# Kernel tuning notes

Hardware: AMD Instinct MI355X
Metric: run time of the kernel (lower is better)

Reference implementation:

```python
import jax, jax.numpy as jnp
import numpy as np

H, DH = 8, 40                      # heads, dim_head
SCALE = DH ** -0.5
NEG = -3.4028235e38                # -finfo(float32).max
EMBDIM, STEPS, EMBEDS = 512, 1000, 50


def _gelu(x):
    return jax.nn.gelu(x, approximate=False)  # torch.nn.GELU default (erf)


def setup_inputs() -> dict:
    key = jax.random.key(0)
    ks = jax.random.split(key, 16)
    b, i, j = 16, 4096, 77
    qd, cd, inner = 320, 768, 320
    s = lambda k, sh, f: jax.random.normal(k, sh, jnp.float32) * f
    bc2 = jnp.tile(jnp.array([0.0, -3.0], jnp.float32), H)  # INITBIAS on class 1
    return dict(
        x=jax.random.normal(ks[0], (b, i, qd), jnp.float32),
        embs=jax.random.normal(ks[1], (b, j, cd), jnp.float32),
        cam=jax.random.uniform(ks[2], (b, i, j), jnp.float32),
        progress=jax.random.uniform(ks[3], (b,), jnp.float32),
        strength=jnp.float32(1.0),
        Wq=s(ks[4], (qd, inner), qd ** -0.5),
        Wk=s(ks[5], (cd, inner), cd ** -0.5),
        Wv=s(ks[6], (cd, inner), cd ** -0.5),
        Wo=s(ks[7], (inner, qd), inner ** -0.5),
        bo=jnp.zeros((qd,), jnp.float32),
        emb1=s(ks[8], (EMBEDS + 1, EMBDIM), 1.0),
        emb2=s(ks[9], (STEPS // EMBEDS, EMBDIM), 1.0),
        Wc1=s(ks[10], (EMBDIM, EMBDIM), EMBDIM ** -0.5),
        bc1=jnp.zeros((EMBDIM,), jnp.float32),
        Wc2=s(ks[11], (EMBDIM, 2 * H), EMBDIM ** -0.5),
        bc2=bc2,
        captiontypes=jax.random.randint(ks[12], (b, j), 0, 5),
    )


def reference(x, embs, cam, progress, strength, Wq, Wk, Wv, Wo, bo,
              emb1, emb2, Wc1, bc1, Wc2, bc2, captiontypes):
    b, i, _ = x.shape
    j = embs.shape[1]
    # projections, split heads: 'b n (h d) -> (b h) n d'
    q = (x @ Wq).reshape(b, i, H, DH).transpose(0, 2, 1, 3).reshape(b * H, i, DH)
    k = (embs @ Wk).reshape(b, j, H, DH).transpose(0, 2, 1, 3).reshape(b * H, j, DH)
    v = (embs @ Wv).reshape(b, j, H, DH).transpose(0, 2, 1, 3).reshape(b * H, j, DH)
    # fp32 QK^T (fp32 already)
    sim = jnp.einsum('bid,bjd->bij', q.astype(jnp.float32), k.astype(jnp.float32))

    # cross_attention_control (CustomCrossAttentionMinimal)
    mask2 = jnp.repeat((captiontypes >= 2)[:, None, :], H, axis=0)  # [(bh),1,j]
    # weight_func under no_grad: std of sim where captiontypes>=2 (unbiased)
    sim_sg = jax.lax.stop_gradient(sim)
    mfull = jnp.broadcast_to(mask2, sim.shape)
    n = mfull.sum().astype(jnp.float32)
    mean = jnp.sum(jnp.where(mfull, sim_sg, 0.0)) / n
    var = jnp.sum(jnp.where(mfull, (sim_sg - mean) ** 2, 0.0)) / (n - 1.0)
    simstd = jnp.sqrt(var)
    wf = jax.lax.stop_gradient(cam * simstd * strength)        # [b,i,j]
    wf = jnp.repeat(wf[:, None], H, axis=1).reshape(b * H, i, j)
    wf = jnp.where(mask2, wf, 0.0)
    useglobal = wf.sum(-1) == 0                                 # [(bh),i]
    wfmax = wf.max(-1, keepdims=True)
    wfb = wf >= (jnp.maximum(wfmax, 0.001) - 0.0001)            # bool [(bh),i,j]
    gmask = jnp.repeat(((captiontypes >= 0) & (captiontypes < 2))[:, None, :], H, axis=0)
    lmask = wfb | (useglobal[:, :, None] & gmask)
    gattn = jax.nn.softmax(jnp.where(gmask, sim, NEG) * SCALE, axis=-1)
    lattn = jax.nn.softmax(jnp.where(lmask, sim, NEG) * SCALE, axis=-1)

    # ProgressClassifier: DiscretizedProgressEmbed -> GELU -> Linear -> GELU -> Linear
    xstep = jnp.minimum(jnp.round(progress * STEPS).astype(jnp.int32), STEPS - 1)
    per = STEPS // EMBEDS  # 20
    e = emb1[xstep // per] + emb2[xstep % per]                  # [b, 512]
    e = _gelu(_gelu(e) @ Wc1 + bc1)
    logits = e @ Wc2 + bc2                                      # [b, 2H]
    pc = jax.nn.softmax(logits.reshape(b, H, 2), axis=-1).reshape(b * H, 2)

    attn = gattn * pc[:, 0, None, None] + lattn * pc[:, 1, None, None]
    out = jnp.einsum('bij,bjd->bid', attn, v.astype(jnp.float32))
    out = out.reshape(b, H, i, DH).transpose(0, 2, 1, 3).reshape(b, i, H * DH)
    return out @ Wo + bo
```

## Files before the change

### kernel.cpp

```cpp
#include <hip/hip_runtime.h>


typedef _Float16 vh8 __attribute__((ext_vector_type(8)));
typedef _Float16 vh4 __attribute__((ext_vector_type(4)));
typedef float    vf4 __attribute__((ext_vector_type(4)));

#define NEGBIG  (-3.4028235e38f)
#define SCALE_F 0.15811388300841897f
#define INFF    (__builtin_inff())

__device__ __forceinline__ vh8 h8zero() {
  vh8 v;
#pragma unroll
  for (int i = 0; i < 8; ++i) v[i] = (_Float16)0.f;
  return v;
}
__device__ __forceinline__ vf4 f4zero() {
  vf4 v;
#pragma unroll
  for (int i = 0; i < 4; ++i) v[i] = 0.f;
  return v;
}
__device__ __forceinline__ float gelu_exact(float x) {
  return 0.5f * x * (1.0f + erff(x * 0.70710678118654752f));
}
__device__ __forceinline__ unsigned swzA(int row) {
  return (unsigned)(((row & 7) << 4) ^ (((row >> 3) & 1) << 5));
}
__device__ __forceinline__ unsigned swzB(int row) {
  return (unsigned)((row & 7) << 4);
}
__device__ __forceinline__ void glds16(const void* g, void* l) {
  __builtin_amdgcn_global_load_lds((const __attribute__((address_space(1))) unsigned*)g,
                                   (__attribute__((address_space(3))) unsigned*)l, 16, 0, 0);
}

__global__ __launch_bounds__(256) void transpose_kernel(
    const float* __restrict__ Wq, const float* __restrict__ Wk,
    const float* __restrict__ Wv, const float* __restrict__ Wo,
    _Float16* __restrict__ WqT, _Float16* __restrict__ WkvT, _Float16* __restrict__ WoT)
{
  __shared__ float ts[32][33];
  int tile = blockIdx.x;
  const float* src; _Float16* dst; int dstK, rowOff;
  if (tile < 100)      { src = Wq; dst = WqT;  dstK = 320; rowOff = 0; }
  else if (tile < 340) { src = Wk; dst = WkvT; dstK = 768; rowOff = 0;   tile -= 100; }
  else if (tile < 580) { src = Wv; dst = WkvT; dstK = 768; rowOff = 320; tile -= 340; }
  else                 { src = Wo; dst = WoT;  dstK = 320; rowOff = 0;   tile -= 580; }
  int kb = tile / 10, nb = tile - kb * 10;
  int k0 = kb * 32, n0 = nb * 32;
  int r = threadIdx.x >> 5, c = threadIdx.x & 31;
#pragma unroll
  for (int p = 0; p < 4; ++p)
    ts[r + p * 8][c] = src[(size_t)(k0 + r + p * 8) * 320 + n0 + c];
  __syncthreads();
#pragma unroll
  for (int p = 0; p < 4; ++p)
    dst[(size_t)(rowOff + n0 + r + p * 8) * dstK + k0 + c] = (_Float16)ts[c][r + p * 8];
}

__global__ __launch_bounds__(256) void vtrans_kernel(
    const _Float16* __restrict__ vf, unsigned* __restrict__ vTg32)
{
  const int b = blockIdx.x, h = blockIdx.y, t = threadIdx.x;
  unsigned* out = vTg32 + (size_t)(b * 8 + h) * 3072;
#pragma unroll
  for (int p = 0; p < 12; ++p) {
    int idx = t + p * 256;
    int d = idx >> 6;
    int u = idx & 63;
    int c = u >> 2, pr = u & 3;
    int sd = (int)(swzA(d) >> 4);
    int j0 = ((c ^ sd) << 3) + pr * 2;
    unsigned lo = 0, hi = 0;
    if (d < 40) {
      if (j0 < 77)     lo = *(const unsigned short*)(vf + (size_t)(b * 77 + j0) * 640 + h * 40 + d);
      if (j0 + 1 < 77) hi = *(const unsigned short*)(vf + (size_t)(b * 77 + j0 + 1) * 640 + h * 40 + d);
    }
    out[idx] = lo | (hi << 16);
  }
}

__global__ __launch_bounds__(256) void kv_gemm_kernel(
    const float* __restrict__ Ap, const _Float16* __restrict__ Bt,
    _Float16* __restrict__ Cp)
{
  const int t = threadIdx.x, lane = t & 63, wave = t >> 6;
  const int m0 = blockIdx.x * 64;
  const int n0 = blockIdx.y * 160;
  const int l15 = lane & 15, l4 = lane >> 4;
  const int rg = wave >> 1, cg = wave & 1;

  vf4 acc[2][5];
#pragma unroll
  for (int a = 0; a < 2; ++a)
#pragma unroll
    for (int bq = 0; bq < 5; ++bq) acc[a][bq] = f4zero();

#pragma unroll 2
  for (int kk = 0; kk < 24; ++kk) {
    int k = kk * 32 + l4 * 8;
    vh8 av[2];
#pragma unroll
    for (int mt = 0; mt < 2; ++mt) {
      int row = m0 + rg * 32 + mt * 16 + l15;
      av[mt] = h8zero();
      if (row < 1232) {
        const float* ap = Ap + (size_t)row * 768 + k;
        float4 f0 = *(const float4*)ap;
        float4 f1 = *(const float4*)(ap + 4);
        vh8 hv;
        hv[0] = (_Float16)f0.x; hv[1] = (_Float16)f0.y; hv[2] = (_Float16)f0.z; hv[3] = (_Float16)f0.w;
        hv[4] = (_Float16)f1.x; hv[5] = (_Float16)f1.y; hv[6] = (_Float16)f1.z; hv[7] = (_Float16)f1.w;
        av[mt] = hv;
      }
    }
#pragma unroll
    for (int nt = 0; nt < 5; ++nt) {
      int n = n0 + cg * 80 + nt * 16 + l15;
      vh8 bv = *(const vh8*)(Bt + (size_t)n * 768 + k);
      acc[0][nt] = __builtin_amdgcn_mfma_f32_16x16x32_f16(av[0], bv, acc[0][nt], 0, 0, 0);
      acc[1][nt] = __builtin_amdgcn_mfma_f32_16x16x32_f16(av[1], bv, acc[1][nt], 0, 0, 0);
    }
  }
#pragma unroll
  for (int mt = 0; mt < 2; ++mt)
#pragma unroll
    for (int nt = 0; nt < 5; ++nt) {
      int n = n0 + cg * 80 + nt * 16 + l15;
#pragma unroll
      for (int r = 0; r < 4; ++r) {
        int m = m0 + rg * 32 + mt * 16 + l4 * 4 + r;
        if (m < 1232) Cp[(size_t)m * 640 + n] = (_Float16)acc[mt][nt][r];
      }
    }
}

__global__ __launch_bounds__(512) void qproj_kernel(
    const float* __restrict__ x, const _Float16* __restrict__ Bt,
    const _Float16* __restrict__ kf, const int* __restrict__ ctypes,
    _Float16* __restrict__ qhm, double* __restrict__ partials)
{
  __shared__ __align__(16) char smem[81920];
  const int t = threadIdx.x, lane = t & 63, wave = t >> 6;
  const int m0 = blockIdx.x * 128;
  const int l15 = lane & 15, l4 = lane >> 4;
  const int wbase = t & ~63;
  const int rg = wave >> 1, cg = wave & 1;
  const float* arow0 = x + (size_t)(m0 + rg * 16 + l15) * 320 + l4 * 8;
  const float* arow1 = x + (size_t)(m0 + 64 + rg * 16 + l15) * 320 + l4 * 8;

  vf4 acc[2][10];
#pragma unroll
  for (int s = 0; s < 2; ++s)
#pragma unroll
    for (int bq = 0; bq < 10; ++bq) acc[s][bq] = f4zero();

  float4 fA[8], fB[8];

#pragma unroll
  for (int p = 0; p < 5; ++p) {
    int idx = t + p * 512;
    int n = idx >> 3, c8 = idx & 7;
    glds16(Bt + (size_t)n * 320 + ((c8 ^ (n & 7)) << 3),
           smem + (size_t)(p * 512 + wbase) * 16);
  }
#pragma unroll
  for (int ks = 0; ks < 2; ++ks) {
    fA[0 + ks * 2 + 0] = *(const float4*)(arow0 + ks * 32);
    fA[0 + ks * 2 + 1] = *(const float4*)(arow0 + ks * 32 + 4);
    fA[4 + ks * 2 + 0] = *(const float4*)(arow1 + ks * 32);
    fA[4 + ks * 2 + 1] = *(const float4*)(arow1 + ks * 32 + 4);
  }
  __syncthreads();

#pragma unroll
  for (int kc = 0; kc < 5; ++kc) {
    char* BsCur = smem + (size_t)(kc & 1) * 40960;
    if (kc < 4) {
      int k0n = (kc + 1) * 64;
      char* BsNxt = smem + (size_t)((kc + 1) & 1) * 40960;
#pragma unroll
      for (int p = 0; p < 5; ++p) {
        int idx = t + p * 512;
        int n = idx >> 3, c8 = idx & 7;
        glds16(Bt + (size_t)n * 320 + k0n + ((c8 ^ (n & 7)) << 3),
               BsNxt + (size_t)(p * 512 + wbase) * 16);
      }
      float4* nxt = (kc & 1) ? fA : fB;
#pragma unroll
      for (int ks = 0; ks < 2; ++ks) {
        nxt[0 + ks * 2 + 0] = *(const float4*)(arow0 + k0n + ks * 32);
        nxt[0 + ks * 2 + 1] = *(const float4*)(arow0 + k0n + ks * 32 + 4);
        nxt[4 + ks * 2 + 0] = *(const float4*)(arow1 + k0n + ks * 32);
        nxt[4 + ks * 2 + 1] = *(const float4*)(arow1 + k0n + ks * 32 + 4);
      }
    }
    float4* cur = (kc & 1) ? fB : fA;
#pragma unroll
    for (int s = 0; s < 2; ++s) {
#pragma unroll
      for (int ks = 0; ks < 2; ++ks) {
        float4 f0 = cur[s * 4 + ks * 2 + 0];
        float4 f1 = cur[s * 4 + ks * 2 + 1];
        vh8 av;
        av[0] = (_Float16)f0.x; av[1] = (_Float16)f0.y; av[2] = (_Float16)f0.z; av[3] = (_Float16)f0.w;
        av[4] = (_Float16)f1.x; av[5] = (_Float16)f1.y; av[6] = (_Float16)f1.z; av[7] = (_Float16)f1.w;
#pragma unroll
        for (int nt = 0; nt < 10; ++nt) {
          int n = cg * 160 + nt * 16 + l15;
          unsigned byte = (unsigned)(n * 128 + (ks * 32 + l4 * 8) * 2) ^ swzB(n);
          vh8 bv = *(const vh8*)(BsCur + byte);
          acc[s][nt] = __builtin_amdgcn_mfma_f32_16x16x32_f16(av, bv, acc[s][nt], 0, 0, 0);
        }
      }
    }
    __syncthreads();
  }

  double S = 0.0, S2 = 0.0;
  const int b = m0 >> 12;
  const int h = wave;
#pragma unroll
  for (int s = 0; s < 2; ++s) {
#pragma unroll
    for (int nt = 0; nt < 10; ++nt) {
      int col = cg * 160 + nt * 16 + l15;
#pragma unroll
      for (int r = 0; r < 4; ++r) {
        int lr = rg * 16 + l4 * 4 + r;
        unsigned byte = (unsigned)(lr * 640 + col * 2) ^ swzB(lr);
        *(_Float16*)(smem + byte) = (_Float16)acc[s][nt][r];
      }
    }
    __syncthreads();
#pragma unroll
    for (int p = 0; p < 5; ++p) {
      int idx = t + p * 512;
      int hh = idx / 320;
      int rem = idx - hh * 320;
      int lrow = rem / 5;
      int c = rem - lrow * 5;
      unsigned sb = (unsigned)(lrow * 640 + hh * 80 + c * 16) ^ swzB(lrow);
      vh8 v = *(const vh8*)(smem + sb);
      int gi = m0 + s * 64 + lrow;
      int bb = gi >> 12, ii = gi & 4095;
      *(vh8*)(qhm + ((size_t)(bb * 8 + hh) * 4096 + ii) * 40 + c * 8) = v;
    }
    {
      vh8 a0v[4], a1v[4];
#pragma unroll
      for (int mt = 0; mt < 4; ++mt) {
        int qrow = mt * 16 + l15;
        unsigned b0 = (unsigned)(qrow * 640 + (h * 40 + l4 * 8) * 2) ^ swzB(qrow);
        a0v[mt] = *(const vh8*)(smem + b0);
        a1v[mt] = h8zero();
        if (l4 == 0) {
          unsigned b1 = (unsigned)(qrow * 640 + (h * 40 + 32) * 2) ^ swzB(qrow);
          a1v[mt] = *(const vh8*)(smem + b1);
        }
      }
#pragma unroll
      for (int jt = 0; jt < 5; ++jt) {
        int j = jt * 16 + l15;
        bool valid = (j < 77);
        vh8 b0 = h8zero(), b1 = h8zero();
        int ctj = -1;
        if (valid) {
          const _Float16* kp = kf + (size_t)(b * 77 + j) * 640 + h * 40;
          b0 = *(const vh8*)(kp + l4 * 8);
          if (l4 == 0) b1 = *(const vh8*)(kp + 32);
          ctj = ctypes[b * 77 + j];
        }
#pragma unroll
        for (int mt = 0; mt < 4; ++mt) {
          vf4 sv4 = f4zero();
          sv4 = __builtin_amdgcn_mfma_f32_16x16x32_f16(a0v[mt], b0, sv4, 0, 0, 0);
          sv4 = __builtin_amdgcn_mfma_f32_16x16x32_f16(a1v[mt], b1, sv4, 0, 0, 0);
          if (ctj >= 2) {
#pragma unroll
            for (int r = 0; r < 4; ++r) {
              double sv = (double)sv4[r];
              S += sv; S2 += sv * sv;
            }
          }
        }
      }
    }
    __syncthreads();
  }
#pragma unroll
  for (int off = 32; off > 0; off >>= 1) {
    S += __shfl_xor(S, off);
    S2 += __shfl_xor(S2, off);
  }
  if (lane == 0) {
    int idx = blockIdx.x * 8 + wave;
    partials[2 * idx + 0] = S;
    partials[2 * idx + 1] = S2;
  }
}

__global__ __launch_bounds__(512) void oproj_kernel(
    const _Float16* __restrict__ hohm, const _Float16* __restrict__ Bt,
    const float* __restrict__ bias, float* __restrict__ out)
{
  __shared__ __align__(16) _Float16 Bs[2][320 * 64];
  const int t = threadIdx.x, lane = t & 63, wave = t >> 6;
  const int m0 = blockIdx.x * 128;
  const int l15 = lane & 15, l4 = lane >> 4;
  const int wbase = t & ~63;
  const int rg = wave >> 1, cg = wave & 1;

  const int gi0 = m0 + rg * 16 + l15;
  const int gi1 = gi0 + 64;
  const int bb0 = gi0 >> 12, ii0 = gi0 & 4095;
  const int bb1 = gi1 >> 12, ii1 = gi1 & 4095;

  vf4 acc[2][10];
#pragma unroll
  for (int s = 0; s < 2; ++s)
#pragma unroll
    for (int bq = 0; bq < 10; ++bq) acc[s][bq] = f4zero();

  vh8 hA[4], hB[4];

#pragma unroll
  for (int p = 0; p < 5; ++p) {
    int idx = t + p * 512;
    int n = idx >> 3, c8 = idx & 7;
    glds16(Bt + (size_t)n * 320 + ((c8 ^ (n & 7)) << 3),
           (char*)Bs[0] + (size_t)(p * 512 + wbase) * 16);
  }
#pragma unroll
  for (int ks = 0; ks < 2; ++ks) {
    int k = ks * 32 + l4 * 8;
    int hh = k / 40, d = k - hh * 40;
    hA[0 + ks] = *(const vh8*)(hohm + ((size_t)(bb0 * 8 + hh) * 4096 + ii0) * 40 + d);
    hA[2 + ks] = *(const vh8*)(hohm + ((size_t)(bb1 * 8 + hh) * 4096 + ii1) * 40 + d);
  }
  __syncthreads();

#pragma unroll
  for (int kc = 0; kc < 5; ++kc) {
    const char* BsCur = (const char*)Bs[kc & 1];
    if (kc < 4) {
      int k0n = (kc + 1) * 64;
      char* BsNxt = (char*)Bs[(kc + 1) & 1];
#pragma unroll
      for (int p = 0; p < 5; ++p) {
        int idx = t + p * 512;
        int n = idx >> 3, c8 = idx & 7;
        glds16(Bt + (size_t)n * 320 + k0n + ((c8 ^ (n & 7)) << 3),
               BsNxt + (size_t)(p * 512 + wbase) * 16);
      }
      vh8* nxt = (kc & 1) ? hA : hB;
#pragma unroll
      for (int ks = 0; ks < 2; ++ks) {
        int k = k0n + ks * 32 + l4 * 8;
        int hh = k / 40, d = k - hh * 40;
        nxt[0 + ks] = *(const vh8*)(hohm + ((size_t)(bb0 * 8 + hh) * 4096 + ii0) * 40 + d);
        nxt[2 + ks] = *(const vh8*)(hohm + ((size_t)(bb1 * 8 + hh) * 4096 + ii1) * 40 + d);
      }
    }
    vh8* cur = (kc & 1) ? hB : hA;
#pragma unroll
    for (int s = 0; s < 2; ++s) {
#pragma unroll
      for (int ks = 0; ks < 2; ++ks) {
#pragma unroll
        for (int nt = 0; nt < 10; ++nt) {
          int n = cg * 160 + nt * 16 + l15;
          unsigned byte = (unsigned)(n * 128 + (ks * 32 + l4 * 8) * 2) ^ swzB(n);
          vh8 bv = *(const vh8*)(BsCur + byte);
          acc[s][nt] = __builtin_amdgcn_mfma_f32_16x16x32_f16(cur[s * 2 + ks], bv, acc[s][nt], 0, 0, 0);
        }
      }
    }
    __syncthreads();
  }
#pragma unroll
  for (int s = 0; s < 2; ++s)
#pragma unroll
    for (int nt = 0; nt < 10; ++nt) {
      int n = cg * 160 + nt * 16 + l15;
      float bias_v = bias[n];
#pragma unroll
      for (int r = 0; r < 4; ++r) {
        int m = m0 + s * 64 + rg * 16 + l4 * 4 + r;
        out[(size_t)m * 320 + n] = acc[s][nt][r] + bias_v;
      }
    }
}

__global__ __launch_bounds__(256) void classifier_kernel(
    const float* __restrict__ progress,
    const float* __restrict__ emb1, const float* __restrict__ emb2,
    const float* __restrict__ Wc1, const float* __restrict__ bc1,
    const float* __restrict__ Wc2, const float* __restrict__ bc2,
    float* __restrict__ pcb)
{
  __shared__ float g[512];
  __shared__ float h1[512];
  __shared__ float lg[16];
  const int b = blockIdx.x;
  const int t = threadIdx.x;

  float pr = progress[b];
  int xstep = (int)rintf(pr * 1000.0f);
  if (xstep > 999) xstep = 999;
  int a = xstep / 20;
  int r = xstep - a * 20;

  for (int d = t; d < 512; d += 256) {
    float e = emb1[a * 512 + d] + emb2[r * 512 + d];
    g[d] = gelu_exact(e);
  }
  __syncthreads();
  for (int n = t; n < 512; n += 256) {
    float acc = bc1[n];
    for (int d = 0; d < 512; ++d) acc = fmaf(g[d], Wc1[d * 512 + n], acc);
    h1[n] = gelu_exact(acc);
  }
  __syncthreads();
  if (t < 16) {
    float acc = bc2[t];
    for (int d = 0; d < 512; ++d) acc = fmaf(h1[d], Wc2[d * 16 + t], acc);
    lg[t] = acc;
  }
  __syncthreads();
  if (t < 8) {
    float a0 = lg[2 * t], a1 = lg[2 * t + 1];
    float mx = fmaxf(a0, a1);
    float e0 = __expf(a0 - mx), e1 = __expf(a1 - mx);
    float inv = 1.0f / (e0 + e1);
    pcb[(b * 8 + t) * 2 + 0] = e0 * inv;
    pcb[(b * 8 + t) * 2 + 1] = e1 * inv;
  }
}

__global__ __launch_bounds__(256) void finalize_kernel(
    const double* __restrict__ partials, const int* __restrict__ ctypes,
    float* __restrict__ ssb)
{
  __shared__ double rs[256];
  __shared__ double rs2[256];
  __shared__ int rc[256];
  const int t = threadIdx.x;
  double S = 0.0, S2 = 0.0;
#pragma unroll
  for (int p = 0; p < 16; ++p) {
    int idx = t + p * 256;
    S += partials[2 * idx + 0];
    S2 += partials[2 * idx + 1];
  }
  int c = 0;
#pragma unroll
  for (int p = 0; p < 5; ++p) {
    int idx = t + p * 256;
    if (idx < 1232) c += (ctypes[idx] >= 2) ? 1 : 0;
  }
  rs[t] = S; rs2[t] = S2; rc[t] = c;
  __syncthreads();
  for (int off = 128; off > 0; off >>= 1) {
    if (t < off) { rs[t] += rs[t + off]; rs2[t] += rs2[t + off]; rc[t] += rc[t + off]; }
    __syncthreads();
  }
  if (t == 0) {
    double n = (double)rc[0] * 8.0 * 4096.0;
    double mean = rs[0] / n;
    double var = (rs2[0] - n * mean * mean) / (n - 1.0);
    ssb[0] = (float)sqrt(var > 0.0 ? var : 0.0);
  }
}

__global__ __launch_bounds__(256) void lmask_kernel(
    const float* __restrict__ cam, const int* __restrict__ ctypes,
    const float* __restrict__ ssb, const float* __restrict__ strengthp,
    unsigned* __restrict__ lmp)
{
  __shared__ float camt[64 * 81];
  __shared__ unsigned char gmv[96];
  __shared__ unsigned char m2v[96];
  const int t = threadIdx.x;
  const int it = blockIdx.x, b = blockIdx.y;
  const int i0 = it * 64;

  if (t < 96) {
    int j = t;
    int ct = (j < 77) ? ctypes[b * 77 + j] : -1;
    gmv[j] = (j < 77 && ct >= 0 && ct < 2) ? 1 : 0;
    m2v[j] = (j < 77 && ct >= 2) ? 1 : 0;
  }
#pragma unroll
  for (int p = 0; p < 20; ++p) {
    int idx = t + p * 256;
    int row = idx / 80;
    int j = idx - row * 80;
    camt[row * 81 + j] = (j < 77) ? cam[((size_t)b * 4096 + i0 + row) * 77 + j] : 0.f;
  }
  __syncthreads();

  const float ss = ssb[0];
  const float st = strengthp[0];
  int row = t >> 2, qd = t & 3;
  float wfv[20];
  float wmax = 0.f, wsum = 0.f;
#pragma unroll
  for (int m = 0; m < 20; ++m) {
    int j = qd + 4 * m;
    float wf = 0.f;
    if (j < 77 && m2v[j]) wf = (camt[row * 81 + j] * ss) * st;
    wfv[m] = wf;
    wmax = fmaxf(wmax, wf);
    wsum += wf;
  }
  wmax = fmaxf(wmax, __shfl_xor(wmax, 1));
  wmax = fmaxf(wmax, __shfl_xor(wmax, 2));
  wsum += __shfl_xor(wsum, 1);
  wsum += __shfl_xor(wsum, 2);
  float thr = fmaxf(wmax, 0.001f) - 0.0001f;
  bool ug = (wsum == 0.f);
  unsigned wbits = 0u;
#pragma unroll
  for (int m = 0; m < 20; ++m) {
    int j = qd + 4 * m;
    bool lv = (wfv[m] >= thr) || (ug && (j < 77) && gmv[j]);
    if (lv) wbits |= (1u << m);
  }
  lmp[((size_t)b * 4096 + i0 + row) * 4 + qd] = wbits;
}

__global__ __launch_bounds__(256) void attn_kernel(
    const _Float16* __restrict__ qhm, const _Float16* __restrict__ kf,
    const unsigned* __restrict__ vTg32, const int* __restrict__ ctypes,
    const float* __restrict__ pcb, const unsigned* __restrict__ lmp,
    _Float16* __restrict__ hohm)
{
  __shared__ _Float16 vT[48 * 128];
  __shared__ _Float16 attnbuf[64 * 128];
  __shared__ __align__(16) _Float16 qt[64 * 40];
  __shared__ unsigned lmw[256];
  __shared__ float gbf[96];
  __shared__ float nbf[96];

  const int t = threadIdx.x, lane = t & 63, wave = t >> 6;
  const int it = blockIdx.x, b = blockIdx.y, h = blockIdx.z;
  const int i0 = it * 64;
  const int l15 = lane & 15, l4 = lane >> 4;

  if (t < 96) {
    int j = t;
    bool valid = (j < 77);
    int ct = valid ? ctypes[b * 77 + j] : -1;
    bool gm = valid && ct >= 0 && ct < 2;
    gbf[j] = gm ? 0.f : (valid ? NEGBIG : -INFF);
    nbf[j] = valid ? NEGBIG : -INFF;
  }
  lmw[t] = lmp[((size_t)b * 4096 + i0) * 4 + t];

  const _Float16* qsrc = qhm + ((size_t)(b * 8 + h) * 4096 + i0) * 40;
  glds16(qsrc + t * 8, (char*)qt + t * 16);
  if (t < 64) glds16(qsrc + (256 + t) * 8, (char*)qt + (256 + t) * 16);

  {
    const unsigned* src0 = vTg32 + (size_t)(b * 8 + h) * 3072;
#pragma unroll
    for (int p = 0; p < 3; ++p) {
      int idx = t + p * 256;
      glds16(src0 + idx * 4, (char*)vT + (size_t)(p * 256 + (t & ~63)) * 16);
    }
  }
#pragma unroll
  for (int p = 0; p < 2; ++p) {
    int idx = t + p * 256;
    int row = idx >> 3, c = idx & 7;
    unsigned byte = (unsigned)(row * 256 + 160 + c * 4) ^ swzA(row);
    *(unsigned*)((char*)attnbuf + byte) = 0u;
  }

  vh8 k0v[5], k1v[5];
#pragma unroll
  for (int jt = 0; jt < 5; ++jt) {
    int j = jt * 16 + l15;
    k0v[jt] = h8zero(); k1v[jt] = h8zero();
    if (j < 77) {
      const _Float16* kp = kf + (size_t)(b * 77 + j) * 640 + h * 40;
      k0v[jt] = *(const vh8*)(kp + l4 * 8);
      if (l4 == 0) k1v[jt] = *(const vh8*)(kp + 32);
    }
  }

  __syncthreads();

  const int myrow = wave * 16 + l15;
  vh8 qf0 = *(const vh8*)((const char*)qt + myrow * 80 + l4 * 16);
  vh8 qf1 = h8zero();
  if (l4 == 0) qf1 = *(const vh8*)((const char*)qt + myrow * 80 + 64);

  vf4 sacc[5];
#pragma unroll
  for (int jt = 0; jt < 5; ++jt) sacc[jt] = f4zero();
#pragma unroll
  for (int jt = 0; jt < 5; ++jt) {
    sacc[jt] = __builtin_amdgcn_mfma_f32_16x16x32_f16(k0v[jt], qf0, sacc[jt], 0, 0, 0);
    sacc[jt] = __builtin_amdgcn_mfma_f32_16x16x32_f16(k1v[jt], qf1, sacc[jt], 0, 0, 0);
  }

  const float pc0 = pcb[(b * 8 + h) * 2 + 0];
  const float pc1 = pcb[(b * 8 + h) * 2 + 1];
  unsigned wbits[4];
#pragma unroll
  for (int r = 0; r < 4; ++r) wbits[r] = lmw[myrow * 4 + r];

  float gv[5][4], lv[5][4];
  float mg = -INFF, ml = -INFF;
#pragma unroll
  for (int jt = 0; jt < 5; ++jt) {
    int jbase = jt * 16 + l4 * 4;
    float4 gb4 = *(const float4*)&gbf[jbase];
    float4 nb4 = *(const float4*)&nbf[jbase];
    const float* gbp = (const float*)&gb4;
    const float* nbp = (const float*)&nb4;
#pragma unroll
    for (int r = 0; r < 4; ++r) {
      float sv = sacc[jt][r];
      float g = fmaf(sv, SCALE_F, gbp[r]);
      unsigned bit = (wbits[r] >> (jt * 4 + l4)) & 1u;
      float l = fmaf(sv, SCALE_F, bit ? 0.f : nbp[r]);
      gv[jt][r] = g; lv[jt][r] = l;
      mg = fmaxf(mg, g); ml = fmaxf(ml, l);
    }
  }
  mg = fmaxf(mg, __shfl_xor(mg, 16)); mg = fmaxf(mg, __shfl_xor(mg, 32));
  ml = fmaxf(ml, __shfl_xor(ml, 16)); ml = fmaxf(ml, __shfl_xor(ml, 32));
  float sG = 0.f, sL = 0.f;
#pragma unroll
  for (int jt = 0; jt < 5; ++jt)
#pragma unroll
    for (int r = 0; r < 4; ++r) {
      float eg = __expf(gv[jt][r] - mg);
      float el = __expf(lv[jt][r] - ml);
      gv[jt][r] = eg; lv[jt][r] = el;
      sG += eg; sL += el;
    }
  sG += __shfl_xor(sG, 16); sG += __shfl_xor(sG, 32);
  sL += __shfl_xor(sL, 16); sL += __shfl_xor(sL, 32);
  float rG = pc0 / sG, rL = pc1 / sL;
  {
    unsigned swz = swzA(myrow);
    unsigned rowbase = (unsigned)(myrow * 256);
#pragma unroll
    for (int jt = 0; jt < 5; ++jt) {
      vh4 w;
#pragma unroll
      for (int r = 0; r < 4; ++r)
        w[r] = (_Float16)fmaf(gv[jt][r], rG, lv[jt][r] * rL);
      unsigned byte = (rowbase + (unsigned)((jt * 16 + l4 * 4) * 2)) ^ swz;
      *(vh4*)((char*)attnbuf + byte) = w;
    }
  }
  __syncthreads();

  vf4 oacc[3];
#pragma unroll
  for (int nt = 0; nt < 3; ++nt) oacc[nt] = f4zero();
#pragma unroll
  for (int ks = 0; ks < 3; ++ks) {
    int arow = wave * 16 + l15;
    unsigned abyte = (unsigned)(arow * 256 + (ks * 32 + l4 * 8) * 2) ^ swzA(arow);
    vh8 pa = *(const vh8*)((const char*)attnbuf + abyte);
#pragma unroll
    for (int nt = 0; nt < 3; ++nt) {
      int n = nt * 16 + l15;
      unsigned byte = (unsigned)(n * 256 + (ks * 32 + l4 * 8) * 2) ^ swzA(n);
      vh8 vb = *(const vh8*)((const char*)vT + byte);
      oacc[nt] = __builtin_amdgcn_mfma_f32_16x16x32_f16(pa, vb, oacc[nt], 0, 0, 0);
    }
  }
#pragma unroll
  for (int nt = 0; nt < 3; ++nt) {
    int d = nt * 16 + l15;
    if (d < 40) {
#pragma unroll
      for (int r = 0; r < 4; ++r) {
        int m = wave * 16 + l4 * 4 + r;
        qt[m * 40 + d] = (_Float16)oacc[nt][r];
      }
    }
  }
  __syncthreads();

  _Float16* obase = hohm + ((size_t)(b * 8 + h) * 4096 + i0) * 40;
  {
    vh8 v = *(const vh8*)((const char*)qt + t * 16);
    *(vh8*)(obase + t * 8) = v;
  }
  if (t < 64) {
    vh8 v = *(const vh8*)((const char*)qt + (256 + t) * 16);
    *(vh8*)(obase + (256 + t) * 8) = v;
  }
}

extern "C" void kernel_launch(void* const* d_in, const int* in_sizes, int n_in,
                              void* d_out, int out_size, void* d_ws, size_t ws_size,
                              hipStream_t stream)
{
  const float* x        = (const float*)d_in[0];
  const float* embs     = (const float*)d_in[1];
  const float* cam      = (const float*)d_in[2];
  const float* progress = (const float*)d_in[3];
  const float* strength = (const float*)d_in[4];
  const float* Wq       = (const float*)d_in[5];
  const float* Wk       = (const float*)d_in[6];
  const float* Wv       = (const float*)d_in[7];
  const float* Wo       = (const float*)d_in[8];
  const float* bo       = (const float*)d_in[9];
  const float* emb1     = (const float*)d_in[10];
  const float* emb2     = (const float*)d_in[11];
  const float* Wc1      = (const float*)d_in[12];
  const float* bc1      = (const float*)d_in[13];
  const float* Wc2      = (const float*)d_in[14];
  const float* bc2      = (const float*)d_in[15];
  const int*   ctypes   = (const int*)d_in[16];

  char* w = (char*)d_ws;
  auto alloc = [&](size_t bytes) { char* p = w; w += (bytes + 255) & ~(size_t)255; return p; };
  _Float16* qhm   = (_Float16*)alloc(65536ull * 320 * 2);
  _Float16* hohm  = (_Float16*)alloc(65536ull * 320 * 2);
  _Float16* kvb   = (_Float16*)alloc(1232ull * 640 * 2);
  unsigned* vTg   = (unsigned*)alloc(128ull * 3072 * 4);
  _Float16* WqT   = (_Float16*)alloc(320ull * 320 * 2);
  _Float16* WkvT  = (_Float16*)alloc(640ull * 768 * 2);
  _Float16* WoT   = (_Float16*)alloc(320ull * 320 * 2);
  unsigned* lmp   = (unsigned*)alloc(65536ull * 4 * 4);
  float*    pcb   = (float*)alloc(256 * 4);
  double*   part  = (double*)alloc(4096ull * 2 * 8);
  float*    ssb   = (float*)alloc(256);

  transpose_kernel<<<680, 256, 0, stream>>>(Wq, Wk, Wv, Wo, WqT, WkvT, WoT);
  classifier_kernel<<<16, 256, 0, stream>>>(progress, emb1, emb2, Wc1, bc1, Wc2, bc2, pcb);
  kv_gemm_kernel<<<dim3(20, 4), 256, 0, stream>>>(embs, WkvT, kvb);
  vtrans_kernel<<<dim3(16, 8), 256, 0, stream>>>(kvb + 320, vTg);
  qproj_kernel<<<512, 512, 0, stream>>>(x, WqT, kvb, ctypes, qhm, part);
  finalize_kernel<<<1, 256, 0, stream>>>(part, ctypes, ssb);
  lmask_kernel<<<dim3(64, 16), 256, 0, stream>>>(cam, ctypes, ssb, strength, lmp);
  attn_kernel<<<dim3(64, 16, 8), 256, 0, stream>>>(qhm, kvb, vTg, ctypes, pcb, lmp, hohm);
  oproj_kernel<<<512, 512, 0, stream>>>(hohm, WoT, bo, (float*)d_out);
}
```

Before: 249.8 us.

## Deepen GEMM prefetch to two stages with explicit vmcnt waits

In both the Q-projection and output-projection GEMM kernels, the next two K-chunks are now kept in flight instead of one. Each buffer is refilled right after its compute finishes, and partial vmcnt waits plus raw s_barrier replace full __syncthreads. The aim is to hide global-load latency behind MFMA work rather than draining every load before each chunk. The hand-counted vmcnt(9) depends on the exact number of outstanding loads the compiler emits per stage, so a miscount could read stale shared memory or data.

```diff
diff --git a/kernel.cpp b/kernel.cpp
--- a/kernel.cpp
+++ b/kernel.cpp
@@ -8,6 +8,10 @@
 #define NEGBIG  (-3.4028235e38f)
 #define SCALE_F 0.15811388300841897f
 #define INFF    (__builtin_inff())
+
+#define WAITCNT9() do { asm volatile("s_waitcnt vmcnt(9)" ::: "memory"); __builtin_amdgcn_sched_barrier(0); } while (0)
+#define WAITCNT0() do { asm volatile("s_waitcnt vmcnt(0)" ::: "memory"); __builtin_amdgcn_sched_barrier(0); } while (0)
+#define SBAR()     __builtin_amdgcn_s_barrier()
 
 __device__ __forceinline__ vh8 h8zero() {
   vh8 v;
@@ -162,7 +166,7 @@
   for (int p = 0; p < 5; ++p) {
     int idx = t + p * 512;
     int n = idx >> 3, c8 = idx & 7;
-    glds16(Bt + (size_t)n * 320 + ((c8 ^ (n & 7)) << 3),
+    glds16(Bt + (size_t)n * 320 + 0 + ((c8 ^ (n & 7)) << 3),
            smem + (size_t)(p * 512 + wbase) * 16);
   }
 #pragma unroll
@@ -172,30 +176,27 @@
     fA[4 + ks * 2 + 0] = *(const float4*)(arow1 + ks * 32);
     fA[4 + ks * 2 + 1] = *(const float4*)(arow1 + ks * 32 + 4);
   }
-  __syncthreads();
+  __builtin_amdgcn_sched_barrier(0);
+#pragma unroll
+  for (int p = 0; p < 5; ++p) {
+    int idx = t + p * 512;
+    int n = idx >> 3, c8 = idx & 7;
+    glds16(Bt + (size_t)n * 320 + 64 + ((c8 ^ (n & 7)) << 3),
+           smem + 40960 + (size_t)(p * 512 + wbase) * 16);
+  }
+#pragma unroll
+  for (int ks = 0; ks < 2; ++ks) {
+    fB[0 + ks * 2 + 0] = *(const float4*)(arow0 + 64 + ks * 32);
+    fB[0 + ks * 2 + 1] = *(const float4*)(arow0 + 64 + ks * 32 + 4);
+    fB[4 + ks * 2 + 0] = *(const float4*)(arow1 + 64 + ks * 32);
+    fB[4 + ks * 2 + 1] = *(const float4*)(arow1 + 64 + ks * 32 + 4);
+  }
+  WAITCNT9();
+  SBAR();
 
 #pragma unroll
   for (int kc = 0; kc < 5; ++kc) {
     char* BsCur = smem + (size_t)(kc & 1) * 40960;
-    if (kc < 4) {
-      int k0n = (kc + 1) * 64;
-      char* BsNxt = smem + (size_t)((kc + 1) & 1) * 40960;
-#pragma unroll
-      for (int p = 0; p < 5; ++p) {
-        int idx = t + p * 512;
-        int n = idx >> 3, c8 = idx & 7;
-        glds16(Bt + (size_t)n * 320 + k0n + ((c8 ^ (n & 7)) << 3),
-               BsNxt + (size_t)(p * 512 + wbase) * 16);
-      }
-      float4* nxt = (kc & 1) ? fA : fB;
-#pragma unroll
-      for (int ks = 0; ks < 2; ++ks) {
-        nxt[0 + ks * 2 + 0] = *(const float4*)(arow0 + k0n + ks * 32);
-        nxt[0 + ks * 2 + 1] = *(const float4*)(arow0 + k0n + ks * 32 + 4);
-        nxt[4 + ks * 2 + 0] = *(const float4*)(arow1 + k0n + ks * 32);
-        nxt[4 + ks * 2 + 1] = *(const float4*)(arow1 + k0n + ks * 32 + 4);
-      }
-    }
     float4* cur = (kc & 1) ? fB : fA;
 #pragma unroll
     for (int s = 0; s < 2; ++s) {
@@ -215,8 +216,32 @@
         }
       }
     }
-    __syncthreads();
-  }
+    if (kc < 4) {
+      SBAR();
+      if (kc < 3) {
+        int k0n = (kc + 2) * 64;
+#pragma unroll
+        for (int p = 0; p < 5; ++p) {
+          int idx = t + p * 512;
+          int n = idx >> 3, c8 = idx & 7;
+          glds16(Bt + (size_t)n * 320 + k0n + ((c8 ^ (n & 7)) << 3),
+                 BsCur + (size_t)(p * 512 + wbase) * 16);
+        }
+#pragma unroll
+        for (int ks = 0; ks < 2; ++ks) {
+          cur[0 + ks * 2 + 0] = *(const float4*)(arow0 + k0n + ks * 32);
+          cur[0 + ks * 2 + 1] = *(const float4*)(arow0 + k0n + ks * 32 + 4);
+          cur[4 + ks * 2 + 0] = *(const float4*)(arow1 + k0n + ks * 32);
+          cur[4 + ks * 2 + 1] = *(const float4*)(arow1 + k0n + ks * 32 + 4);
+        }
+        WAITCNT9();
+      } else {
+        WAITCNT0();
+      }
+      SBAR();
+    }
+  }
+  __syncthreads();
 
   double S = 0.0, S2 = 0.0;
   const int b = m0 >> 12;
@@ -329,7 +354,7 @@
   for (int p = 0; p < 5; ++p) {
     int idx = t + p * 512;
     int n = idx >> 3, c8 = idx & 7;
-    glds16(Bt + (size_t)n * 320 + ((c8 ^ (n & 7)) << 3),
+    glds16(Bt + (size_t)n * 320 + 0 + ((c8 ^ (n & 7)) << 3),
            (char*)Bs[0] + (size_t)(p * 512 + wbase) * 16);
   }
 #pragma unroll
@@ -339,30 +364,27 @@
     hA[0 + ks] = *(const vh8*)(hohm + ((size_t)(bb0 * 8 + hh) * 4096 + ii0) * 40 + d);
     hA[2 + ks] = *(const vh8*)(hohm + ((size_t)(bb1 * 8 + hh) * 4096 + ii1) * 40 + d);
   }
-  __syncthreads();
+  __builtin_amdgcn_sched_barrier(0);
+#pragma unroll
+  for (int p = 0; p < 5; ++p) {
+    int idx = t + p * 512;
+    int n = idx >> 3, c8 = idx & 7;
+    glds16(Bt + (size_t)n * 320 + 64 + ((c8 ^ (n & 7)) << 3),
+           (char*)Bs[1] + (size_t)(p * 512 + wbase) * 16);
+  }
+#pragma unroll
+  for (int ks = 0; ks < 2; ++ks) {
+    int k = 64 + ks * 32 + l4 * 8;
+    int hh = k / 40, d = k - hh * 40;
+    hB[0 + ks] = *(const vh8*)(hohm + ((size_t)(bb0 * 8 + hh) * 4096 + ii0) * 40 + d);
+    hB[2 + ks] = *(const vh8*)(hohm + ((size_t)(bb1 * 8 + hh) * 4096 + ii1) * 40 + d);
+  }
+  WAITCNT9();
+  SBAR();
 
 #pragma unroll
   for (int kc = 0; kc < 5; ++kc) {
-    const char* BsCur = (const char*)Bs[kc & 1];
-    if (kc < 4) {
-      int k0n = (kc + 1) * 64;
-      char* BsNxt = (char*)Bs[(kc + 1) & 1];
-#pragma unroll
-      for (int p = 0; p < 5; ++p) {
-        int idx = t + p * 512;
-        int n = idx >> 3, c8 = idx & 7;
-        glds16(Bt + (size_t)n * 320 + k0n + ((c8 ^ (n & 7)) << 3),
-               BsNxt + (size_t)(p * 512 + wbase) * 16);
-      }
-      vh8* nxt = (kc & 1) ? hA : hB;
-#pragma unroll
-      for (int ks = 0; ks < 2; ++ks) {
-        int k = k0n + ks * 32 + l4 * 8;
-        int hh = k / 40, d = k - hh * 40;
-        nxt[0 + ks] = *(const vh8*)(hohm + ((size_t)(bb0 * 8 + hh) * 4096 + ii0) * 40 + d);
-        nxt[2 + ks] = *(const vh8*)(hohm + ((size_t)(bb1 * 8 + hh) * 4096 + ii1) * 40 + d);
-      }
-    }
+    char* BsCur = (char*)Bs[kc & 1];
     vh8* cur = (kc & 1) ? hB : hA;
 #pragma unroll
     for (int s = 0; s < 2; ++s) {
@@ -377,7 +399,30 @@
         }
       }
     }
-    __syncthreads();
+    if (kc < 4) {
+      SBAR();
+      if (kc < 3) {
+        int k0n = (kc + 2) * 64;
+#pragma unroll
+        for (int p = 0; p < 5; ++p) {
+          int idx = t + p * 512;
+          int n = idx >> 3, c8 = idx & 7;
+          glds16(Bt + (size_t)n * 320 + k0n + ((c8 ^ (n & 7)) << 3),
+                 BsCur + (size_t)(p * 512 + wbase) * 16);
+        }
+#pragma unroll
+        for (int ks = 0; ks < 2; ++ks) {
+          int k = k0n + ks * 32 + l4 * 8;
+          int hh = k / 40, d = k - hh * 40;
+          cur[0 + ks] = *(const vh8*)(hohm + ((size_t)(bb0 * 8 + hh) * 4096 + ii0) * 40 + d);
+          cur[2 + ks] = *(const vh8*)(hohm + ((size_t)(bb1 * 8 + hh) * 4096 + ii1) * 40 + d);
+        }
+        WAITCNT9();
+      } else {
+        WAITCNT0();
+      }
+      SBAR();
+    }
   }
 #pragma unroll
   for (int s = 0; s < 2; ++s)
```

After: 251.8 us. About the same (+0.8%).
